# Performance work log

Measured on AMD Instinct MI355X. Metric: run time of the kernel, lower is better.

Reference implementation:

```python
import jax, jax.numpy as jnp
import numpy as np

EPS = 1e-5

def _ste(x, q):
    # straight-through estimator: forward=q, backward=identity
    return x + jax.lax.stop_gradient(q - x)

def act_quant(x):
    # per-token int8 absmax quantization (BitNet b1.58 style), fake-quantized
    scale = 127.0 / jnp.clip(jnp.max(jnp.abs(x), axis=-1, keepdims=True), EPS)
    q = jnp.clip(jnp.round(x * scale), -128.0, 127.0) / scale
    return _ste(x, q)

def weight_quant(w):
    # ternary {-1,0,1} weights scaled by mean absolute value
    s = jnp.clip(jnp.mean(jnp.abs(w)), EPS)
    q = jnp.clip(jnp.round(w / s), -1.0, 1.0) * s
    return _ste(w, q)

def bit_linear(x, w):
    # x: [..., in], w: [out, in]
    return jnp.einsum('bsi,oi->bso', act_quant(x), weight_quant(w))

def setup_inputs() -> dict:
    key = jax.random.key(0)
    k1, k2, k3 = jax.random.split(key, 3)
    d_model, hidden = 2048, 4 * 2048
    x = jax.random.normal(k1, (4, 2048, d_model), dtype=jnp.float32)
    w1 = jax.random.normal(k2, (hidden, d_model), dtype=jnp.float32) * 0.02
    w2 = jax.random.normal(k3, (d_model, hidden), dtype=jnp.float32) * 0.02
    return {"x": x, "w1": w1, "w2": w2}

def reference(x, w1, w2):
    h = bit_linear(x, w1)            # [B, S, 4*d]
    h = jax.nn.gelu(h, approximate=False)  # exact erf GELU (nn.GELU default)
    return bit_linear(h, w2)         # [B, S, d]
```

## Files before the change

kernel.cpp:

```cpp
#include <hip/hip_runtime.h>
#include <hip/hip_bf16.h>
#include <hip/hip_fp16.h>
#include <stdint.h>

#define TPB 256
#define EPSF 1e-5f

using i32x4 = __attribute__((ext_vector_type(4))) int;


__device__ __forceinline__ void gload16(const void* g, void* l) {
    __builtin_amdgcn_global_load_lds(
        (__attribute__((address_space(1))) void*)g,
        (__attribute__((address_space(3))) void*)l,
        16, 0, 0);
}

__device__ __forceinline__ float wave_reduce_sum(float v) {
#pragma unroll
    for (int off = 32; off > 0; off >>= 1) v += __shfl_down(v, off, 64);
    return v;
}

__device__ __forceinline__ float wave_reduce_max(float v) {
#pragma unroll
    for (int off = 32; off > 0; off >>= 1) v = fmaxf(v, __shfl_down(v, off, 64));
    return v;
}

__device__ __forceinline__ int q8(float f, float scale, float lo, float hi) {
    return (int)fminf(fmaxf(rintf(f * scale), lo), hi);
}


__global__ void abssum_partial(const float* __restrict__ w, int n4,
                               float* __restrict__ part) {
    const float4* w4 = (const float4*)w;
    float acc = 0.f;
    for (int i = blockIdx.x * TPB + threadIdx.x; i < n4; i += gridDim.x * TPB) {
        float4 v = w4[i];
        acc += fabsf(v.x) + fabsf(v.y) + fabsf(v.z) + fabsf(v.w);
    }
    acc = wave_reduce_sum(acc);
    __shared__ float sh[4];
    if ((threadIdx.x & 63) == 0) sh[threadIdx.x >> 6] = acc;
    __syncthreads();
    if (threadIdx.x == 0) part[blockIdx.x] = sh[0] + sh[1] + sh[2] + sh[3];
}

__global__ void finalize_scales(const float* __restrict__ part1,
                                const float* __restrict__ part2,
                                float* __restrict__ scales, int nparts, float inv_n) {
    float a = 0.f, b = 0.f;
    for (int i = threadIdx.x; i < nparts; i += TPB) { a += part1[i]; b += part2[i]; }
    a = wave_reduce_sum(a);
    b = wave_reduce_sum(b);
    __shared__ float sa[4], sb[4];
    if ((threadIdx.x & 63) == 0) { sa[threadIdx.x >> 6] = a; sb[threadIdx.x >> 6] = b; }
    __syncthreads();
    if (threadIdx.x == 0) {
        scales[0] = fmaxf((sa[0] + sa[1] + sa[2] + sa[3]) * inv_n, EPSF);
        scales[1] = fmaxf((sb[0] + sb[1] + sb[2] + sb[3]) * inv_n, EPSF);
    }
}


__global__ void quant_w_i8(const float* __restrict__ w,
                           signed char* __restrict__ wq,
                           const float* __restrict__ scales, int sidx, int n4) {
    const float inv = 1.0f / scales[sidx];
    const float4* w4 = (const float4*)w;
    unsigned* oq = (unsigned*)wq;
    for (int i = blockIdx.x * TPB + threadIdx.x; i < n4; i += gridDim.x * TPB) {
        float4 v = w4[i];
        unsigned p = ((unsigned)(q8(v.x, inv, -1.f, 1.f) & 0xff)) |
                     ((unsigned)(q8(v.y, inv, -1.f, 1.f) & 0xff) << 8) |
                     ((unsigned)(q8(v.z, inv, -1.f, 1.f) & 0xff) << 16) |
                     ((unsigned)(q8(v.w, inv, -1.f, 1.f) & 0xff) << 24);
        oq[i] = p;
    }
}


template <int NF4>
__global__ void quant_x_i8(const float* __restrict__ in,
                           signed char* __restrict__ outq,
                           float* __restrict__ dq, int cols) {
    const long long row = blockIdx.x;
    const float4* r4 = (const float4*)(in + row * (long long)cols);
    float4 v[NF4];
    float mx = 0.f;
#pragma unroll
    for (int j = 0; j < NF4; ++j) {
        v[j] = r4[threadIdx.x + TPB * j];
        mx = fmaxf(mx, fmaxf(fmaxf(fabsf(v[j].x), fabsf(v[j].y)),
                             fmaxf(fabsf(v[j].z), fabsf(v[j].w))));
    }
    mx = wave_reduce_max(mx);
    __shared__ float sh[4];
    __shared__ float res;
    if ((threadIdx.x & 63) == 0) sh[threadIdx.x >> 6] = mx;
    __syncthreads();
    if (threadIdx.x == 0) res = fmaxf(fmaxf(sh[0], sh[1]), fmaxf(sh[2], sh[3]));
    __syncthreads();
    const float clipped = fmaxf(res, EPSF);
    const float scale = 127.f / clipped;
    if (threadIdx.x == 0) dq[row] = clipped / 127.f;
    unsigned* oq = (unsigned*)(outq + row * (long long)cols);
#pragma unroll
    for (int j = 0; j < NF4; ++j) {
        unsigned p = ((unsigned)(q8(v[j].x, scale, -128.f, 127.f) & 0xff)) |
                     ((unsigned)(q8(v[j].y, scale, -128.f, 127.f) & 0xff) << 8) |
                     ((unsigned)(q8(v[j].z, scale, -128.f, 127.f) & 0xff) << 16) |
                     ((unsigned)(q8(v[j].w, scale, -128.f, 127.f) & 0xff) << 24);
        oq[threadIdx.x + TPB * j] = p;
    }
}


template <int NJ>
__global__ void quant_h_i8(const unsigned short* __restrict__ h,
                           signed char* __restrict__ outq,
                           float* __restrict__ dq, int cols) {
    const long long row = blockIdx.x;
    const unsigned short* rp = h + row * (long long)cols;
    uint4 v[NJ];
    float mx = 0.f;
#pragma unroll
    for (int j = 0; j < NJ; ++j) {
        v[j] = *(const uint4*)(rp + (threadIdx.x + TPB * j) * 8);
        const unsigned* u = (const unsigned*)&v[j];
#pragma unroll
        for (int e = 0; e < 4; ++e) {
            float2 f2 = __half22float2(*(const __half2*)&u[e]);
            mx = fmaxf(mx, fmaxf(fabsf(f2.x), fabsf(f2.y)));
        }
    }
    mx = wave_reduce_max(mx);
    __shared__ float sh[4];
    __shared__ float res;
    if ((threadIdx.x & 63) == 0) sh[threadIdx.x >> 6] = mx;
    __syncthreads();
    if (threadIdx.x == 0) res = fmaxf(fmaxf(sh[0], sh[1]), fmaxf(sh[2], sh[3]));
    __syncthreads();
    const float clipped = fmaxf(res, EPSF);
    const float scale = 127.f / clipped;
    if (threadIdx.x == 0) dq[row] = clipped / 127.f;
    uint2* oq = (uint2*)(outq + row * (long long)cols);
#pragma unroll
    for (int j = 0; j < NJ; ++j) {
        const unsigned* u = (const unsigned*)&v[j];
        unsigned o[2] = {0, 0};
#pragma unroll
        for (int e = 0; e < 4; ++e) {
            float2 f2 = __half22float2(*(const __half2*)&u[e]);
            unsigned b0 = (unsigned)(q8(f2.x, scale, -128.f, 127.f) & 0xff);
            unsigned b1 = (unsigned)(q8(f2.y, scale, -128.f, 127.f) & 0xff);
            o[e >> 1] |= (b0 | (b1 << 8)) << ((e & 1) * 16);
        }
        oq[threadIdx.x + TPB * j] = *(uint2*)o;
    }
}


__device__ __forceinline__ void stage_half(const char* Xb, long long rowB, int prow,
                                           int tk, char* dst, int tid, int cbs) {
    const long long gc = (long long)tk * 128 + cbs;
    const int r = tid >> 3;
    gload16(Xb + (long long)(prow + r) * rowB + gc, dst + tid * 16);
    gload16(Xb + (long long)(prow + 64 + r) * rowB + gc, dst + 8192 + tid * 16);
}

#define QUAD(MB, NB)                                                            \
    _Pragma("unroll") for (int mi = 0; mi < 4; ++mi)                            \
    _Pragma("unroll") for (int ni = 0; ni < 2; ++ni)                            \
    _Pragma("unroll") for (int ks = 0; ks < 2; ++ks)                            \
        acc[(MB)*4 + mi][(NB)*2 + ni] = __builtin_amdgcn_mfma_i32_16x16x64_i8(  \
            aq[mi][ks], bq[(NB)*2 + ni][ks], acc[(MB)*4 + mi][(NB)*2 + ni], 0, 0, 0);

template <int OUT>
__global__ __launch_bounds__(512, 2) void gemm8p_i8(
    const signed char* __restrict__ A, const signed char* __restrict__ B,
    void* __restrict__ Cv, int N, int K,
    const float* __restrict__ dq, const float* __restrict__ scales, int sidx) {
    __shared__ __align__(16) char lds[131072];

    const int tid = threadIdx.x;
    const int lane = tid & 63;
    const int wid = tid >> 6;
    const int wr = wid >> 2;
    const int wc = wid & 3;

    const unsigned gx = gridDim.x;
    unsigned lin = blockIdx.y * gx + blockIdx.x;
    const unsigned qq = (gx * gridDim.y) >> 3;
    lin = (lin & 7) * qq + (lin >> 3);
    const unsigned bx = lin % gx;
    const unsigned by = lin / gx;

    const long long M0 = (long long)by * 256;
    const long long N0 = (long long)bx * 256;
    const long long rb = (long long)K;
    const char* Ab = (const char*)A + M0 * rb;
    const char* Bb = (const char*)B + N0 * rb;
    const int nt = K >> 7;

    const int cbs = (((tid & 7) ^ ((tid >> 3) & 7)) << 4);

    const int l15 = lane & 15, l4 = lane >> 4;
    const int swz = (lane & 7) << 4;
    const int acb0 = (l4 * 16) ^ swz;
    const int acb1 = (64 + l4 * 16) ^ swz;
    const int aoff = wr * 16384;
    const int boff = 32768 + (wc >> 1) * 16384 + (wc & 1) * 8192;

    i32x4 acc[8][4] = {};
    i32x4 aq[4][2], bq[4][2];

    stage_half(Bb, rb, 0,   0, lds + 32768,         tid, cbs);
    stage_half(Bb, rb, 128, 0, lds + 32768 + 16384, tid, cbs);
    stage_half(Ab, rb, 0,   0, lds + 0,             tid, cbs);
    stage_half(Ab, rb, 128, 0, lds + 16384,         tid, cbs);
    if (nt > 1) {
        stage_half(Bb, rb, 0,   1, lds + 65536 + 32768,         tid, cbs);
        stage_half(Bb, rb, 128, 1, lds + 65536 + 32768 + 16384, tid, cbs);
        stage_half(Ab, rb, 0,   1, lds + 65536,                 tid, cbs);
        asm volatile("s_waitcnt vmcnt(6)" ::: "memory");
    } else {
        asm volatile("s_waitcnt vmcnt(0)" ::: "memory");
    }
    __builtin_amdgcn_sched_barrier(0);
    __builtin_amdgcn_s_barrier();

    for (int t = 0; t < nt; ++t) {
        char* cur = lds + ((t & 1) << 16);
        char* nxt = lds + (((t + 1) & 1) << 16);
        const bool s1 = (t + 1) < nt;
        const bool s2 = (t + 2) < nt;

#pragma unroll
        for (int mi = 0; mi < 4; ++mi) {
            const char* p = cur + aoff + (mi * 16 + l15) * 128;
            aq[mi][0] = *(const i32x4*)(p + acb0);
            aq[mi][1] = *(const i32x4*)(p + acb1);
        }
#pragma unroll
        for (int ni = 0; ni < 4; ++ni) {
            const char* p = cur + boff + (ni * 16 + l15) * 128;
            bq[ni][0] = *(const i32x4*)(p + acb0);
            bq[ni][1] = *(const i32x4*)(p + acb1);
        }
        if (s1) stage_half(Ab, rb, 128, t + 1, nxt + 16384, tid, cbs);
        __builtin_amdgcn_s_setprio(1);
        QUAD(0, 0);
        __builtin_amdgcn_s_setprio(0);
        __builtin_amdgcn_s_barrier();

        if (s2) stage_half(Bb, rb, 0, t + 2, cur + 32768, tid, cbs);
        __builtin_amdgcn_s_setprio(1);
        QUAD(0, 1);
        __builtin_amdgcn_s_setprio(0);
        __builtin_amdgcn_s_barrier();

#pragma unroll
        for (int mi = 0; mi < 4; ++mi) {
            const char* p = cur + aoff + ((mi + 4) * 16 + l15) * 128;
            aq[mi][0] = *(const i32x4*)(p + acb0);
            aq[mi][1] = *(const i32x4*)(p + acb1);
        }
        if (s2) stage_half(Bb, rb, 128, t + 2, cur + 32768 + 16384, tid, cbs);
        __builtin_amdgcn_s_setprio(1);
        QUAD(1, 0);
        __builtin_amdgcn_s_setprio(0);
        __builtin_amdgcn_s_barrier();

        if (s2) stage_half(Ab, rb, 0, t + 2, cur, tid, cbs);
        __builtin_amdgcn_s_setprio(1);
        QUAD(1, 1);
        __builtin_amdgcn_s_setprio(0);
        if (s2) { asm volatile("s_waitcnt vmcnt(6)" ::: "memory"); }
        else    { asm volatile("s_waitcnt vmcnt(0)" ::: "memory"); }
        __builtin_amdgcn_sched_barrier(0);
        __builtin_amdgcn_s_barrier();
    }

    const float s = scales[sidx];
#pragma unroll
    for (int mi = 0; mi < 8; ++mi) {
#pragma unroll
        for (int r = 0; r < 4; ++r) {
            const long long m = M0 + wr * 128 + mi * 16 + l4 * 4 + r;
            const float f = dq[m] * s;
#pragma unroll
            for (int ni = 0; ni < 4; ++ni) {
                const long long n = N0 + wc * 64 + ni * 16 + l15;
                float v = (float)acc[mi][ni][r] * f;
                if (OUT) {
                    v = 0.5f * v * (1.0f + erff(v * 0.70710678118654752440f));
                    __half hh = __float2half(v);
                    __builtin_nontemporal_store(
                        *(const unsigned short*)&hh,
                        (unsigned short*)Cv + m * (long long)N + n);
                } else {
                    __builtin_nontemporal_store(
                        v, (float*)Cv + m * (long long)N + n);
                }
            }
        }
    }
}


extern "C" void kernel_launch(void* const* d_in, const int* in_sizes, int n_in,
                              void* d_out, int out_size, void* d_ws, size_t ws_size,
                              hipStream_t stream) {
    (void)n_in; (void)out_size;
    const float* x  = (const float*)d_in[0];
    const float* w1 = (const float*)d_in[1];
    const float* w2 = (const float*)d_in[2];
    float* out = (float*)d_out;

    const int D = 2048, H = 8192;
    const long long M = (long long)in_sizes[0] / D;

    char* base = (char*)d_ws;
    size_t off = 0;
    auto alloc = [&](size_t bytes) -> char* {
        char* r = base + off;
        off = (off + bytes + 255) & ~(size_t)255;
        return r;
    };

    const bool fullM = ws_size >= (size_t)236 * 1024 * 1024;
    const long long MC = fullM ? M : M / 2;

    float* part1 = (float*)alloc(2048 * 4);
    float* part2 = (float*)alloc(2048 * 4);
    float* scales = (float*)alloc(256);
    float* dqx = (float*)alloc((size_t)M * 4);
    float* dqh = (float*)alloc((size_t)M * 4);
    signed char* wq = (signed char*)alloc((size_t)H * D);
    signed char* xq = (signed char*)alloc((size_t)M * D);
    signed char* hq = (signed char*)alloc((size_t)M * H);
    unsigned short* hf = (unsigned short*)alloc((size_t)MC * H * 2);

    const int nw4 = H * D / 4;
    abssum_partial<<<2048, TPB, 0, stream>>>(w1, nw4, part1);
    abssum_partial<<<2048, TPB, 0, stream>>>(w2, nw4, part2);
    finalize_scales<<<1, TPB, 0, stream>>>(part1, part2, scales, 2048,
                                           1.0f / (float)(H * D));
    quant_w_i8<<<2048, TPB, 0, stream>>>(w1, wq, scales, 0, nw4);
    quant_x_i8<2><<<(int)M, TPB, 0, stream>>>(x, xq, dqx, D);

    if (fullM) {
        gemm8p_i8<1><<<dim3(H / 256, (int)(M / 256)), 512, 0, stream>>>(
            xq, wq, hf, H, D, dqx, scales, 0);
        quant_h_i8<4><<<(int)M, TPB, 0, stream>>>(hf, hq, dqh, H);
    } else {
        for (int g = 0; g < 2; ++g) {
            const long long m0 = g * MC;
            gemm8p_i8<1><<<dim3(H / 256, (int)(MC / 256)), 512, 0, stream>>>(
                xq + m0 * D, wq, hf, H, D, dqx + m0, scales, 0);
            quant_h_i8<4><<<(int)MC, TPB, 0, stream>>>(hf, hq + m0 * H, dqh + m0, H);
        }
    }

    quant_w_i8<<<2048, TPB, 0, stream>>>(w2, wq, scales, 1, nw4);

    gemm8p_i8<0><<<dim3(D / 256, (int)(M / 256)), 512, 0, stream>>>(
        hq, wq, out, D, H, dqh, scales, 1);
}
```

Before: 408.1 us.

## Make first GEMM persistent over M tiles and use tanh-form GELU

The first GEMM now launches a fixed 32x8 grid in which each block walks several M tiles for its N column, continuing the software pipeline across tile boundaries and emitting the epilogue every 16 K-steps. This is meant to hide prologue/epilogue load latency and keep the weight panel hot. It also replaces exact erf GELU with a tanh-approximation built on exp2 and a hardware reciprocal, which is cheaper but introduces small numeric deviation before the fp16 store and requantization. The second GEMM is specialized without the template.

```diff
diff --git a/kernel.cpp b/kernel.cpp
--- a/kernel.cpp
+++ b/kernel.cpp
@@ -30,6 +30,13 @@
 
 __device__ __forceinline__ int q8(float f, float scale, float lo, float hi) {
     return (int)fminf(fmaxf(rintf(f * scale), lo), hi);
+}
+
+__device__ __forceinline__ float gelu_fast(float x) {
+    float x2 = x * x;
+    float u = x * (0.7978845608f + 0.0356774081f * x2);
+    float e = exp2f(u * -2.8853900817779268f);
+    return x * __builtin_amdgcn_rcpf(1.0f + e);
 }
 
 
@@ -178,11 +185,139 @@
         acc[(MB)*4 + mi][(NB)*2 + ni] = __builtin_amdgcn_mfma_i32_16x16x64_i8(  \
             aq[mi][ks], bq[(NB)*2 + ni][ks], acc[(MB)*4 + mi][(NB)*2 + ni], 0, 0, 0);
 
-template <int OUT>
-__global__ __launch_bounds__(512, 2) void gemm8p_i8(
+
+__global__ __launch_bounds__(512, 2) void gemm1p(
     const signed char* __restrict__ A, const signed char* __restrict__ B,
-    void* __restrict__ Cv, int N, int K,
-    const float* __restrict__ dq, const float* __restrict__ scales, int sidx) {
+    unsigned short* __restrict__ C, int N, int K,
+    const float* __restrict__ dq, const float* __restrict__ scales, int ntile) {
+    __shared__ __align__(16) char lds[131072];
+
+    const int tid = threadIdx.x;
+    const int lane = tid & 63;
+    const int wid = tid >> 6;
+    const int wr = wid >> 2;
+    const int wc = wid & 3;
+
+    const unsigned gx = gridDim.x;
+    unsigned lin = blockIdx.y * gx + blockIdx.x;
+    const unsigned qq = (gx * gridDim.y) >> 3;
+    lin = (lin & 7) * qq + (lin >> 3);
+    const unsigned bx = lin % gx;
+    const unsigned byg = lin / gx;
+
+    const int n0 = (int)bx * 256;
+    const long long rb = (long long)K;
+    const char* Ab = (const char*)A;
+    const char* Bb = (const char*)B;
+
+    const int NTT = ntile << 4;
+
+    const int cbs = (((tid & 7) ^ ((tid >> 3) & 7)) << 4);
+    const int l15 = lane & 15, l4 = lane >> 4;
+    const int swz = (lane & 7) << 4;
+    const int acb0 = (l4 * 16) ^ swz;
+    const int acb1 = (64 + l4 * 16) ^ swz;
+    const int aoff = wr * 16384;
+    const int boff = 32768 + (wc >> 1) * 16384 + (wc & 1) * 8192;
+
+    i32x4 acc[8][4] = {};
+    i32x4 aq[4][2], bq[4][2];
+
+    auto mrow = [&](int v) -> int { return ((int)byg * ntile + (v >> 4)) * 256; };
+
+    stage_half(Bb, rb, n0, 0, lds + 32768, tid, cbs);
+    stage_half(Bb, rb, n0 + 128, 0, lds + 32768 + 16384, tid, cbs);
+    stage_half(Ab, rb, mrow(0), 0, lds + 0, tid, cbs);
+    stage_half(Ab, rb, mrow(0) + 128, 0, lds + 16384, tid, cbs);
+    stage_half(Bb, rb, n0, 1, lds + 65536 + 32768, tid, cbs);
+    stage_half(Bb, rb, n0 + 128, 1, lds + 65536 + 32768 + 16384, tid, cbs);
+    stage_half(Ab, rb, mrow(1), 1, lds + 65536, tid, cbs);
+    asm volatile("s_waitcnt vmcnt(6)" ::: "memory");
+    __builtin_amdgcn_sched_barrier(0);
+    __builtin_amdgcn_s_barrier();
+
+    const float s = scales[0];
+
+    for (int vt = 0; vt < NTT; ++vt) {
+        char* cur = lds + ((vt & 1) << 16);
+        char* nxt = lds + (((vt + 1) & 1) << 16);
+        const bool s1 = (vt + 1) < NTT;
+        const bool s2 = (vt + 2) < NTT;
+        const int k1 = (vt + 1) & 15;
+        const int k2 = (vt + 2) & 15;
+
+#pragma unroll
+        for (int mi = 0; mi < 4; ++mi) {
+            const char* p = cur + aoff + (mi * 16 + l15) * 128;
+            aq[mi][0] = *(const i32x4*)(p + acb0);
+            aq[mi][1] = *(const i32x4*)(p + acb1);
+        }
+#pragma unroll
+        for (int ni = 0; ni < 4; ++ni) {
+            const char* p = cur + boff + (ni * 16 + l15) * 128;
+            bq[ni][0] = *(const i32x4*)(p + acb0);
+            bq[ni][1] = *(const i32x4*)(p + acb1);
+        }
+        if (s1) stage_half(Ab, rb, mrow(vt + 1) + 128, k1, nxt + 16384, tid, cbs);
+        __builtin_amdgcn_s_setprio(1);
+        QUAD(0, 0);
+        __builtin_amdgcn_s_setprio(0);
+        __builtin_amdgcn_s_barrier();
+
+        if (s2) stage_half(Bb, rb, n0, k2, cur + 32768, tid, cbs);
+        __builtin_amdgcn_s_setprio(1);
+        QUAD(0, 1);
+        __builtin_amdgcn_s_setprio(0);
+        __builtin_amdgcn_s_barrier();
+
+#pragma unroll
+        for (int mi = 0; mi < 4; ++mi) {
+            const char* p = cur + aoff + ((mi + 4) * 16 + l15) * 128;
+            aq[mi][0] = *(const i32x4*)(p + acb0);
+            aq[mi][1] = *(const i32x4*)(p + acb1);
+        }
+        if (s2) stage_half(Bb, rb, n0 + 128, k2, cur + 32768 + 16384, tid, cbs);
+        __builtin_amdgcn_s_setprio(1);
+        QUAD(1, 0);
+        __builtin_amdgcn_s_setprio(0);
+        __builtin_amdgcn_s_barrier();
+
+        if (s2) stage_half(Ab, rb, mrow(vt + 2), k2, cur, tid, cbs);
+        __builtin_amdgcn_s_setprio(1);
+        QUAD(1, 1);
+        __builtin_amdgcn_s_setprio(0);
+        if (s2) { asm volatile("s_waitcnt vmcnt(6)" ::: "memory"); }
+        else    { asm volatile("s_waitcnt vmcnt(0)" ::: "memory"); }
+        __builtin_amdgcn_sched_barrier(0);
+        __builtin_amdgcn_s_barrier();
+
+        if ((vt & 15) == 15) {
+            const int m0 = mrow(vt);
+#pragma unroll
+            for (int mi = 0; mi < 8; ++mi) {
+#pragma unroll
+                for (int r = 0; r < 4; ++r) {
+                    const long long m = m0 + wr * 128 + mi * 16 + l4 * 4 + r;
+                    const float f = dq[m] * s;
+#pragma unroll
+                    for (int ni = 0; ni < 4; ++ni) {
+                        const long long n = n0 + wc * 64 + ni * 16 + l15;
+                        float v = gelu_fast((float)acc[mi][ni][r] * f);
+                        __half hh = __float2half(v);
+                        C[m * (long long)N + n] = *(const unsigned short*)&hh;
+                        acc[mi][ni][r] = 0;
+                    }
+                }
+            }
+        }
+    }
+}
+
+
+__global__ __launch_bounds__(512, 2) void gemm2k(
+    const signed char* __restrict__ A, const signed char* __restrict__ B,
+    float* __restrict__ C, int N, int K,
+    const float* __restrict__ dq, const float* __restrict__ scales) {
     __shared__ __align__(16) char lds[131072];
 
     const int tid = threadIdx.x;
@@ -206,7 +341,6 @@
     const int nt = K >> 7;
 
     const int cbs = (((tid & 7) ^ ((tid >> 3) & 7)) << 4);
-
     const int l15 = lane & 15, l4 = lane >> 4;
     const int swz = (lane & 7) << 4;
     const int acb0 = (l4 * 16) ^ swz;
@@ -221,14 +355,10 @@
     stage_half(Bb, rb, 128, 0, lds + 32768 + 16384, tid, cbs);
     stage_half(Ab, rb, 0,   0, lds + 0,             tid, cbs);
     stage_half(Ab, rb, 128, 0, lds + 16384,         tid, cbs);
-    if (nt > 1) {
-        stage_half(Bb, rb, 0,   1, lds + 65536 + 32768,         tid, cbs);
-        stage_half(Bb, rb, 128, 1, lds + 65536 + 32768 + 16384, tid, cbs);
-        stage_half(Ab, rb, 0,   1, lds + 65536,                 tid, cbs);
-        asm volatile("s_waitcnt vmcnt(6)" ::: "memory");
-    } else {
-        asm volatile("s_waitcnt vmcnt(0)" ::: "memory");
-    }
+    stage_half(Bb, rb, 0,   1, lds + 65536 + 32768,         tid, cbs);
+    stage_half(Bb, rb, 128, 1, lds + 65536 + 32768 + 16384, tid, cbs);
+    stage_half(Ab, rb, 0,   1, lds + 65536,                 tid, cbs);
+    asm volatile("s_waitcnt vmcnt(6)" ::: "memory");
     __builtin_amdgcn_sched_barrier(0);
     __builtin_amdgcn_s_barrier();
 
@@ -284,7 +414,7 @@
         __builtin_amdgcn_s_barrier();
     }
 
-    const float s = scales[sidx];
+    const float s = scales[1];
 #pragma unroll
     for (int mi = 0; mi < 8; ++mi) {
 #pragma unroll
@@ -294,17 +424,8 @@
 #pragma unroll
             for (int ni = 0; ni < 4; ++ni) {
                 const long long n = N0 + wc * 64 + ni * 16 + l15;
-                float v = (float)acc[mi][ni][r] * f;
-                if (OUT) {
-                    v = 0.5f * v * (1.0f + erff(v * 0.70710678118654752440f));
-                    __half hh = __float2half(v);
-                    __builtin_nontemporal_store(
-                        *(const unsigned short*)&hh,
-                        (unsigned short*)Cv + m * (long long)N + n);
-                } else {
-                    __builtin_nontemporal_store(
-                        v, (float*)Cv + m * (long long)N + n);
-                }
+                __builtin_nontemporal_store(
+                    (float)acc[mi][ni][r] * f, C + m * (long long)N + n);
             }
         }
     }
@@ -353,20 +474,19 @@
     quant_x_i8<2><<<(int)M, TPB, 0, stream>>>(x, xq, dqx, D);
 
     if (fullM) {
-        gemm8p_i8<1><<<dim3(H / 256, (int)(M / 256)), 512, 0, stream>>>(
-            xq, wq, hf, H, D, dqx, scales, 0);
+        gemm1p<<<dim3(32, 8), 512, 0, stream>>>(xq, wq, hf, H, D, dqx, scales, 4);
         quant_h_i8<4><<<(int)M, TPB, 0, stream>>>(hf, hq, dqh, H);
     } else {
         for (int g = 0; g < 2; ++g) {
             const long long m0 = g * MC;
-            gemm8p_i8<1><<<dim3(H / 256, (int)(MC / 256)), 512, 0, stream>>>(
-                xq + m0 * D, wq, hf, H, D, dqx + m0, scales, 0);
+            gemm1p<<<dim3(32, 8), 512, 0, stream>>>(
+                xq + m0 * D, wq, hf, H, D, dqx + m0, scales, 2);
             quant_h_i8<4><<<(int)MC, TPB, 0, stream>>>(hf, hq + m0 * H, dqh + m0, H);
         }
     }
 
     quant_w_i8<<<2048, TPB, 0, stream>>>(w2, wq, scales, 1, nw4);
 
-    gemm8p_i8<0><<<dim3(D / 256, (int)(M / 256)), 512, 0, stream>>>(
-        hq, wq, out, D, H, dqh, scales, 1);
-}
+    gemm2k<<<dim3(D / 256, (int)(M / 256)), 512, 0, stream>>>(
+        hq, wq, out, D, H, dqh, scales);
+}
```

Result: faster. 369.8 us (-9.4%).
